# Optimization experiments

Hardware: AMD Instinct MI355X
Metric: run time of the kernel (lower is better)

## Reference

```python
import jax, jax.numpy as jnp
import numpy as np

B, S, DM = 4, 2048, 1024
H, HD = 16, 64  # num_heads, head_dimension


def setup_inputs() -> dict:
    key = jax.random.key(0)
    ks = jax.random.split(key, 11)
    s = 0.02
    return {
        "queries": jax.random.normal(ks[0], (B, S, DM), dtype=jnp.float32),
        "keys": jax.random.normal(ks[1], (B, S, DM), dtype=jnp.float32),
        "values": jax.random.normal(ks[2], (B, S, DM), dtype=jnp.float32),
        # projection params, stored [in, out] (transpose of torch Linear weight)
        "Wq": jax.random.normal(ks[3], (DM, H * HD), dtype=jnp.float32) * s,
        "bq": jnp.zeros((H * HD,), dtype=jnp.float32),
        "Wk": jax.random.normal(ks[4], (DM, H * HD), dtype=jnp.float32) * s,
        "bk": jnp.zeros((H * HD,), dtype=jnp.float32),
        "Wv": jax.random.normal(ks[5], (DM, H * HD), dtype=jnp.float32) * s,
        "bv": jnp.zeros((H * HD,), dtype=jnp.float32),
        "Wo": jax.random.normal(ks[6], (H * HD, DM), dtype=jnp.float32) * s,
        "bo": jnp.zeros((DM,), dtype=jnp.float32),
    }


def reference(queries, keys, values, Wq, bq, Wk, bk, Wv, bv, Wo, bo):
    b, s, _ = queries.shape
    # project and split heads: [b, s, H*HD] -> [b, H, s, HD]
    def split(x):
        return x.reshape(b, s, H, HD).transpose(0, 2, 1, 3)
    q = split(queries @ Wq + bq)
    k = split(keys @ Wk + bk)
    v = split(values @ Wv + bv)
    # raw scores [b, H, sq, sk]
    attn = jnp.einsum("bhqd,bhkd->bhqk", q, k)
    # FAITHFUL to source: mask is a no-op (masked_fill result discarded);
    # softmax over axis=2 (the QUERY axis), then scaled by 1/sqrt(HD) after.
    attn = jax.nn.softmax(attn, axis=2) / jnp.sqrt(jnp.float32(HD))
    out = jnp.einsum("bhqk,bhkd->bhqd", attn, v)  # [b, H, s, HD]
    out = out.transpose(0, 2, 1, 3).reshape(b, s, H * HD)
    return out @ Wo + bo
```

## Files before the change

### kernel.cpp

```cpp
#include <hip/hip_runtime.h>
#include <cstddef>


typedef unsigned short u16t;
typedef __attribute__((ext_vector_type(8))) short short8;
typedef __attribute__((ext_vector_type(4))) float floatx4;
typedef __attribute__((ext_vector_type(4))) unsigned int uintx4;

#define MFMA16(a, b, c) __builtin_amdgcn_mfma_f32_16x16x32_bf16((a), (b), (c), 0, 0, 0)
#define GLDS16(g, l)                                                        \
  __builtin_amdgcn_global_load_lds(                                         \
      (const __attribute__((address_space(1))) unsigned int*)(g),           \
      (__attribute__((address_space(3))) unsigned int*)(l), 16, 0, 0)

#if __has_builtin(__builtin_amdgcn_exp2f)
#define EXP2(x) __builtin_amdgcn_exp2f(x)
#else
#define EXP2(x) __expf(0.69314718f * (x))
#endif

static __device__ __forceinline__ u16t f2bf(float f) {
  union { float f; unsigned u; } v; v.f = f;
  unsigned r = v.u + 0x7FFFu + ((v.u >> 16) & 1u);
  return (u16t)(r >> 16);
}
static __device__ __forceinline__ unsigned pack2(float hi, float lo) {
  union { float f; unsigned u; } a, b; a.f = hi; b.f = lo;
  return __builtin_amdgcn_perm(a.u + 0x8000u, b.u + 0x8000u, 0x07060302u);
}
static __device__ __forceinline__ unsigned cvtpk(float lo, float hi) {
  unsigned r;
  asm("v_cvt_pk_bf16_f32 %0, %1, %2" : "=v"(r) : "v"(lo), "v"(hi));
  return r;
}

static __device__ __forceinline__ int swz(int row, int col) {
  return (((col >> 3) ^ (row & 7)) << 3) | (col & 7);
}

#define SEQ    2048
#define NHEAD  16
#define HDIM   64
#define DMODEL 1024

__global__ __launch_bounds__(256)
void wt_kernel(const float* __restrict__ W0, const float* __restrict__ W1,
               const float* __restrict__ W2, const float* __restrict__ W3,
               u16t* __restrict__ T0, u16t* __restrict__ T1,
               u16t* __restrict__ T2, u16t* __restrict__ T3) {
  int id = blockIdx.x * 256 + threadIdx.x;
  int wsel = id >> 17;
  int r = id & 131071;
  int n = r & 1023;
  int k0 = (r >> 10) << 3;
  const float* W = wsel == 0 ? W0 : wsel == 1 ? W1 : wsel == 2 ? W2 : W3;
  u16t* T = wsel == 0 ? T0 : wsel == 1 ? T1 : wsel == 2 ? T2 : T3;
  const float* src = W + (size_t)k0 * 1024 + n;
  float f[8];
#pragma unroll
  for (int i = 0; i < 8; ++i) f[i] = src[(size_t)i * 1024];
  uint4 p;
  p.x = pack2(f[1], f[0]); p.y = pack2(f[3], f[2]);
  p.z = pack2(f[5], f[4]); p.w = pack2(f[7], f[6]);
  *(uint4*)&T[(size_t)n * 1024 + (k0 & ~63) + swz(n, k0 & 63)] = p;
}

__global__ __launch_bounds__(256)
void cvt_kernel(const float* __restrict__ X0, const float* __restrict__ X1,
                u16t* __restrict__ T0, u16t* __restrict__ T1) {
  int id = blockIdx.x * 256 + threadIdx.x;
  int wsel = id >> 20;
  int r = id & 1048575;
  int m = r >> 7;
  int k0 = (r & 127) << 3;
  const float* X = wsel == 0 ? X0 : X1;
  u16t* T = wsel == 0 ? T0 : T1;
  const float4* src = (const float4*)(X + (size_t)m * 1024 + k0);
  float4 a = src[0], b = src[1];
  uint4 p;
  p.x = pack2(a.y, a.x); p.y = pack2(a.w, a.z);
  p.z = pack2(b.y, b.x); p.w = pack2(b.w, b.z);
  *(uint4*)&T[(size_t)m * 1024 + (k0 & ~63) + swz(m, k0 & 63)] = p;
}

template <int MODE>
__global__ __launch_bounds__(256)
void gemm_bt(const void* __restrict__ Ap0, const void* __restrict__ Ap1,
             const u16t* __restrict__ BT0, const u16t* __restrict__ BT1,
             const float* __restrict__ bias0, const float* __restrict__ bias1,
             void* __restrict__ Cp0, void* __restrict__ Cp1,
             float sc0, float sc1, const float* __restrict__ sscv) {
  constexpr int K = 1024;
  __shared__ __align__(16) u16t lA[128 * 64];
  __shared__ __align__(16) u16t lB[128 * 64];
  const int z = blockIdx.z;
  const void* Ap = z ? Ap1 : Ap0;
  const u16t* BT = z ? BT1 : BT0;
  const float* bias = z ? bias1 : bias0;
  void* Cp = z ? Cp1 : Cp0;
  const float qsc = z ? sc1 : sc0;
  const int tid = threadIdx.x;
  const int lane = tid & 63, w = tid >> 6;
  const int wm = w >> 1, wn = w & 1;
  const int lrow = lane & 15, lq = lane >> 4;
  const int raw = blockIdx.y * 8 + blockIdx.x;
  const int xcd = raw & 7, slot = raw >> 3;
  const int m0 = (xcd * 8 + (slot >> 3)) * 128;
  const int n0 = (slot & 7) * 128;

  floatx4 acc[4][4];
#pragma unroll
  for (int i = 0; i < 4; ++i)
#pragma unroll
    for (int j = 0; j < 4; ++j) acc[i][j] = {0.f, 0.f, 0.f, 0.f};

  for (int kb = 0; kb < K; kb += 64) {
    if constexpr (MODE == 2) {
      const float* Ag = (const float*)Ap;
#pragma unroll
      for (int i = 0; i < 8; ++i) {
        int e = (i * 256 + tid) * 4;
        int r = e >> 6, c = e & 63;
        const float* src = Ag + (size_t)(m0 + r) * K + kb + c;
        uint2 p;
        p.x = pack2(src[1], src[0]);
        p.y = pack2(src[3], src[2]);
        *(uint2*)&lA[r * 64 + swz(r, c)] = p;
      }
    } else {
      const u16t* Ag = (const u16t*)Ap;
#pragma unroll
      for (int i = 0; i < 4; ++i) {
        int chunk = w * 4 + i;
        int off = chunk * 1024 + lane * 16;
        int r = off >> 7, ib = off & 127;
        GLDS16(Ag + (size_t)(m0 + r) * K + kb + (ib >> 1), &lA[chunk * 512]);
      }
    }
#pragma unroll
    for (int i = 0; i < 4; ++i) {
      int chunk = w * 4 + i;
      int off = chunk * 1024 + lane * 16;
      int r = off >> 7, ib = off & 127;
      GLDS16(BT + (size_t)(n0 + r) * K + kb + (ib >> 1), &lB[chunk * 512]);
    }
    __syncthreads();
#pragma unroll
    for (int kk = 0; kk < 2; ++kk) {
      short8 af[4], bfr[4];
#pragma unroll
      for (int t = 0; t < 4; ++t) {
        int ar = wm * 64 + t * 16 + lrow;
        af[t] = *(const short8*)&lA[ar * 64 + swz(ar, kk * 32 + lq * 8)];
      }
#pragma unroll
      for (int t = 0; t < 4; ++t) {
        int br = wn * 64 + t * 16 + lrow;
        bfr[t] = *(const short8*)&lB[br * 64 + swz(br, kk * 32 + lq * 8)];
      }
#pragma unroll
      for (int i = 0; i < 4; ++i)
#pragma unroll
        for (int j = 0; j < 4; ++j)
          acc[i][j] = MFMA16(af[i], bfr[j], acc[i][j]);
    }
    __syncthreads();
  }

  float bvv[4];
#pragma unroll
  for (int j = 0; j < 4; ++j) bvv[j] = bias[n0 + wn * 64 + j * 16 + lrow];
  const int h = (n0 + wn * 64) >> 6;
#pragma unroll
  for (int i = 0; i < 4; ++i) {
#pragma unroll
    for (int r = 0; r < 4; ++r) {
      int rg = m0 + wm * 64 + i * 16 + lq * 4 + r;
      int b = rg >> 11, s = rg & 2047;
      float rs;
      if constexpr (MODE == 2) rs = sscv[(size_t)(b * NHEAD + h) * SEQ + s];
      else                     rs = qsc;
#pragma unroll
      for (int j = 0; j < 4; ++j) {
        int cg = n0 + wn * 64 + j * 16 + lrow;
        float v = acc[i][j][r] + bvv[j];
        if constexpr (MODE == 1) {
          ((float*)Cp)[(size_t)rg * 1024 + cg] = v;
        } else {
          v *= rs;
          int d = cg & 63;
          size_t bh = (size_t)(b * NHEAD + h);
          if constexpr (MODE == 0) {
            ((u16t*)Cp)[(bh * SEQ + s) * HDIM + swz(s, d)] = f2bf(v);
          } else {
            int sp = (s & ~31) | (((s >> 2) & 3) << 3) | (s & 3) |
                     (((s >> 4) & 1) << 2);
            ((u16t*)Cp)[(bh * HDIM + d) * SEQ + (s & ~127) + swz(d, sp & 127)] =
                f2bf(v);
          }
        }
      }
    }
  }
}

__global__ __launch_bounds__(256)
void stats_kernel(const u16t* __restrict__ Qb, const u16t* __restrict__ Kb,
                  float* __restrict__ ss) {
  __shared__ __align__(16) u16t lK[8192];
  __shared__ __align__(16) u16t lQ[2][8192];
  const int tid = threadIdx.x, lane = tid & 63, w = tid >> 6;
  const int lrow = lane & 15, lq = lane >> 4;
  const int bh = blockIdx.x;
  const int c0 = blockIdx.y * 128;
  const u16t* Kbase = Kb + (size_t)bh * (SEQ * HDIM);
  const u16t* Qbase = Qb + (size_t)bh * (SEQ * HDIM);

  auto stageQ = [&](int t) {
    u16t* dst = lQ[t & 1];
#pragma unroll
    for (int i = 0; i < 4; ++i) {
      int chunk = w * 4 + i;
      GLDS16(Qbase + ((size_t)t << 13) + chunk * 512 + lane * 8, &dst[chunk * 512]);
    }
  };

#pragma unroll
  for (int i = 0; i < 4; ++i) {
    int chunk = w * 4 + i;
    GLDS16(Kbase + (size_t)c0 * HDIM + chunk * 512 + lane * 8, &lK[chunk * 512]);
  }
  stageQ(0);
  stageQ(1);
  asm volatile("s_waitcnt vmcnt(4)" ::: "memory");
  __builtin_amdgcn_s_barrier();

  short8 bfK[4];
#pragma unroll
  for (int nt = 0; nt < 2; ++nt) {
    int kr = w * 32 + nt * 16 + lrow;
    bfK[nt * 2]     = *(const short8*)&lK[kr * 64 + swz(kr, lq * 8)];
    bfK[nt * 2 + 1] = *(const short8*)&lK[kr * 64 + swz(kr, lq * 8 + 32)];
  }

  float lcur[2] = {0.f, 0.f};

#pragma unroll 2
  for (int it = 0; it < 16; ++it) {
    const u16t* Q_ = lQ[it & 1];
#pragma unroll
    for (int mt = 0; mt < 8; ++mt) {
      int qr = mt * 16 + lrow;
      short8 af0 = *(const short8*)&Q_[qr * 64 + swz(qr, lq * 8)];
      short8 af1 = *(const short8*)&Q_[qr * 64 + swz(qr, lq * 8 + 32)];
#pragma unroll
      for (int nt = 0; nt < 2; ++nt) {
        floatx4 a = {0.f, 0.f, 0.f, 0.f};
        __builtin_amdgcn_s_setprio(1);
        a = MFMA16(af0, bfK[nt * 2], a);
        a = MFMA16(af1, bfK[nt * 2 + 1], a);
        __builtin_amdgcn_s_setprio(0);
        lcur[nt] += (EXP2(a[0]) + EXP2(a[1])) + (EXP2(a[2]) + EXP2(a[3]));
      }
    }
    asm volatile("s_waitcnt lgkmcnt(0)" ::: "memory");
    __builtin_amdgcn_s_barrier();
    if (it < 14) stageQ(it + 2);
    if (it < 15) {
      if (it == 14) asm volatile("s_waitcnt vmcnt(0)" ::: "memory");
      else          asm volatile("s_waitcnt vmcnt(4)" ::: "memory");
      __builtin_amdgcn_s_barrier();
    }
  }
#pragma unroll
  for (int t = 0; t < 2; ++t) {
    float ll = lcur[t];
    ll += __shfl_xor(ll, 16);
    ll += __shfl_xor(ll, 32);
    lcur[t] = ll;
  }
  if (lane < 16) {
#pragma unroll
    for (int t = 0; t < 2; ++t) {
      int col = c0 + w * 32 + t * 16 + lane;
      ss[(size_t)bh * SEQ + col] = 1.f / (8.f * lcur[t]);
    }
  }
}

__global__ __launch_bounds__(256)
void attn_kernel(const u16t* __restrict__ Qb, const u16t* __restrict__ Kb,
                 const u16t* __restrict__ Vt, u16t* __restrict__ Hout) {
  __shared__ __align__(16) u16t sK[2][8192];
  __shared__ __align__(16) u16t sV[2][8192];
  const int tid = threadIdx.x, lane = tid & 63, w = tid >> 6;
  const int lrow = lane & 15, lq = lane >> 4;
  const int bh = blockIdx.x, q0 = blockIdx.y * 256;
  const size_t hb = (size_t)bh * (SEQ * HDIM);

  auto stage = [&](int t) {
    u16t* dK = sK[t & 1];
    u16t* dV = sV[t & 1];
    const int k0 = t << 7;
#pragma unroll
    for (int i = 0; i < 4; ++i) {
      int chunk = w * 4 + i;
      GLDS16(Kb + hb + (size_t)k0 * HDIM + chunk * 512 + lane * 8, &dK[chunk * 512]);
    }
#pragma unroll
    for (int i = 0; i < 4; ++i) {
      int chunk = w * 4 + i;
      int off = chunk * 1024 + lane * 16;
      int d = off >> 8, ib = off & 255;
      GLDS16(Vt + hb + ((size_t)d << 11) + k0 + (ib >> 1), &dV[chunk * 512]);
    }
  };

  u16t* qs = (u16t*)sK;
#pragma unroll
  for (int i = 0; i < 8; ++i) {
    int chunk = w * 8 + i;
    GLDS16(Qb + hb + (size_t)q0 * HDIM + chunk * 512 + lane * 8, &qs[chunk * 512]);
  }
  __syncthreads();
  short8 bq[4][2];
#pragma unroll
  for (int j = 0; j < 4; ++j) {
    int qr = w * 64 + j * 16 + lrow;
    bq[j][0] = *(const short8*)&qs[qr * 64 + swz(qr, lq * 8)];
    bq[j][1] = *(const short8*)&qs[qr * 64 + swz(qr, lq * 8 + 32)];
  }
  __syncthreads();

  floatx4 ao[4][4];
#pragma unroll
  for (int j = 0; j < 4; ++j)
#pragma unroll
    for (int t = 0; t < 4; ++t) ao[j][t] = {0.f, 0.f, 0.f, 0.f};

  stage(0);
  stage(1);

#pragma unroll 2
  for (int kt = 0; kt < 16; ++kt) {
    if (kt < 15) asm volatile("s_waitcnt vmcnt(8)" ::: "memory");
    else         asm volatile("s_waitcnt vmcnt(0)" ::: "memory");
    __builtin_amdgcn_s_barrier();
    const u16t* K_ = sK[kt & 1];
    const u16t* V_ = sV[kt & 1];

#pragma unroll
    for (int kw = 0; kw < 4; ++kw) {
      short8 ak[2][2];
#pragma unroll
      for (int t = 0; t < 2; ++t) {
        int kr = (kw * 2 + t) * 16 + lrow;
        ak[t][0] = *(const short8*)&K_[kr * 64 + swz(kr, lq * 8)];
        ak[t][1] = *(const short8*)&K_[kr * 64 + swz(kr, lq * 8 + 32)];
      }
      short8 pa[4];
#pragma unroll
      for (int j = 0; j < 4; ++j) {
        floatx4 s0 = {0.f, 0.f, 0.f, 0.f}, s1 = {0.f, 0.f, 0.f, 0.f};
        __builtin_amdgcn_s_setprio(1);
        s0 = MFMA16(ak[0][0], bq[j][0], s0);
        s0 = MFMA16(ak[0][1], bq[j][1], s0);
        s1 = MFMA16(ak[1][0], bq[j][0], s1);
        s1 = MFMA16(ak[1][1], bq[j][1], s1);
        __builtin_amdgcn_s_setprio(0);
        uintx4 pw;
        pw[0] = cvtpk(EXP2(s0[0]), EXP2(s0[1]));
        pw[1] = cvtpk(EXP2(s0[2]), EXP2(s0[3]));
        pw[2] = cvtpk(EXP2(s1[0]), EXP2(s1[1]));
        pw[3] = cvtpk(EXP2(s1[2]), EXP2(s1[3]));
        pa[j] = __builtin_bit_cast(short8, pw);
      }
      __builtin_amdgcn_s_setprio(1);
#pragma unroll
      for (int dt = 0; dt < 4; ++dt) {
        int vr = dt * 16 + lrow;
        short8 bv = *(const short8*)&V_[vr * 128 + swz(vr, kw * 32 + lq * 8)];
#pragma unroll
        for (int j = 0; j < 4; ++j)
          ao[j][dt] = MFMA16(pa[j], bv, ao[j][dt]);
      }
      __builtin_amdgcn_s_setprio(0);
    }

    asm volatile("s_waitcnt lgkmcnt(0)" ::: "memory");
    __builtin_amdgcn_s_barrier();
    if (kt < 14) stage(kt + 2);
  }

  const int b = bh >> 4, h = bh & 15;
#pragma unroll
  for (int j = 0; j < 4; ++j)
#pragma unroll
    for (int dt = 0; dt < 4; ++dt) {
      int d = dt * 16 + lrow;
#pragma unroll
      for (int r = 0; r < 4; ++r) {
        int q = q0 + w * 64 + j * 16 + lq * 4 + r;
        Hout[((size_t)b * SEQ + q) * DMODEL + h * HDIM + swz(q, d)] = f2bf(ao[j][dt][r]);
      }
    }
}

extern "C" void kernel_launch(void* const* d_in, const int* in_sizes, int n_in,
                              void* d_out, int out_size, void* d_ws, size_t ws_size,
                              hipStream_t stream) {
  (void)in_sizes; (void)n_in; (void)out_size; (void)ws_size;
  const float* queries = (const float*)d_in[0];
  const float* keys    = (const float*)d_in[1];
  const float* values  = (const float*)d_in[2];
  const float* Wq = (const float*)d_in[3];
  const float* bq = (const float*)d_in[4];
  const float* Wk = (const float*)d_in[5];
  const float* bk = (const float*)d_in[6];
  const float* Wv = (const float*)d_in[7];
  const float* bv = (const float*)d_in[8];
  const float* Wo = (const float*)d_in[9];
  const float* bo = (const float*)d_in[10];

  char* ws = (char*)d_ws;
  const size_t MB = 1024 * 1024;
  u16t* Qb   = (u16t*)(ws + 0 * MB);
  u16t* Kb   = (u16t*)(ws + 16 * MB);
  u16t* qcv  = (u16t*)(ws + 32 * MB);
  u16t* Hout = qcv;
  u16t* kcv  = (u16t*)(ws + 48 * MB);
  u16t* Vt   = kcv;
  u16t* wqt  = (u16t*)(ws + 64 * MB);
  u16t* wkt  = (u16t*)(ws + 66 * MB);
  u16t* wvt  = (u16t*)(ws + 68 * MB);
  u16t* wot  = (u16t*)(ws + 70 * MB);
  float* ssc = (float*)(ws + 72 * MB);

  wt_kernel<<<2048, 256, 0, stream>>>(Wq, Wk, Wv, Wo, wqt, wkt, wvt, wot);

  cvt_kernel<<<8192, 256, 0, stream>>>(queries, keys, qcv, kcv);

  gemm_bt<0><<<dim3(8, 64, 2), 256, 0, stream>>>(
      qcv, kcv, wqt, wkt, bq, bk, Qb, Kb, 1.44269504f, 1.0f, nullptr);

  stats_kernel<<<dim3(64, 16), 256, 0, stream>>>(Qb, Kb, ssc);

  gemm_bt<2><<<dim3(8, 64, 1), 256, 0, stream>>>(
      values, values, wvt, wvt, bv, bv, Vt, Vt, 1.0f, 1.0f, ssc);

  attn_kernel<<<dim3(64, 8), 256, 0, stream>>>(Qb, Kb, Vt, Hout);

  gemm_bt<1><<<dim3(8, 64, 1), 256, 0, stream>>>(
      Hout, Hout, wot, wot, bo, bo, d_out, d_out, 1.0f, 1.0f, nullptr);
}
```

Measured before the change: 400.5 us.

## Prefetch K/V fragments in attention loop and simplify stats kernel staging

The attention kernel now double-buffers its per-step K and V register fragments, loading the next kw slice from LDS while MFMAs run on the current one, and asks for two waves per SIMD through launch bounds. The stats kernel drops its double-buffered async Q staging and priority hints in favour of a single buffer loaded synchronously with __syncthreads. This halves the stats kernel's LDS use, which may raise occupancy, but that kernel can no longer overlap Q loads with compute. The added fragment registers may also strain the register cap that the launch-bounds change imposes on attn_kernel.

```diff
diff --git a/kernel.cpp b/kernel.cpp
--- a/kernel.cpp
+++ b/kernel.cpp
@@ -207,8 +207,8 @@
 __global__ __launch_bounds__(256)
 void stats_kernel(const u16t* __restrict__ Qb, const u16t* __restrict__ Kb,
                   float* __restrict__ ss) {
-  __shared__ __align__(16) u16t lK[8192];
-  __shared__ __align__(16) u16t lQ[2][8192];
+  __shared__ __align__(16) u16t lK[128 * 64];
+  __shared__ __align__(16) u16t lQ[128 * 64];
   const int tid = threadIdx.x, lane = tid & 63, w = tid >> 6;
   const int lrow = lane & 15, lq = lane >> 4;
   const int bh = blockIdx.x;
@@ -216,61 +216,44 @@
   const u16t* Kbase = Kb + (size_t)bh * (SEQ * HDIM);
   const u16t* Qbase = Qb + (size_t)bh * (SEQ * HDIM);
 
-  auto stageQ = [&](int t) {
-    u16t* dst = lQ[t & 1];
-#pragma unroll
-    for (int i = 0; i < 4; ++i) {
-      int chunk = w * 4 + i;
-      GLDS16(Qbase + ((size_t)t << 13) + chunk * 512 + lane * 8, &dst[chunk * 512]);
-    }
-  };
-
 #pragma unroll
   for (int i = 0; i < 4; ++i) {
     int chunk = w * 4 + i;
     GLDS16(Kbase + (size_t)c0 * HDIM + chunk * 512 + lane * 8, &lK[chunk * 512]);
   }
-  stageQ(0);
-  stageQ(1);
-  asm volatile("s_waitcnt vmcnt(4)" ::: "memory");
-  __builtin_amdgcn_s_barrier();
 
   short8 bfK[4];
-#pragma unroll
-  for (int nt = 0; nt < 2; ++nt) {
-    int kr = w * 32 + nt * 16 + lrow;
-    bfK[nt * 2]     = *(const short8*)&lK[kr * 64 + swz(kr, lq * 8)];
-    bfK[nt * 2 + 1] = *(const short8*)&lK[kr * 64 + swz(kr, lq * 8 + 32)];
-  }
-
   float lcur[2] = {0.f, 0.f};
 
-#pragma unroll 2
-  for (int it = 0; it < 16; ++it) {
-    const u16t* Q_ = lQ[it & 1];
+  for (int q0 = 0; q0 < SEQ; q0 += 128) {
+#pragma unroll
+    for (int i = 0; i < 4; ++i) {
+      int chunk = w * 4 + i;
+      GLDS16(Qbase + (size_t)q0 * HDIM + chunk * 512 + lane * 8, &lQ[chunk * 512]);
+    }
+    __syncthreads();
+    if (q0 == 0) {
+#pragma unroll
+      for (int nt = 0; nt < 2; ++nt) {
+        int kr = w * 32 + nt * 16 + lrow;
+        bfK[nt * 2]     = *(const short8*)&lK[kr * 64 + swz(kr, lq * 8)];
+        bfK[nt * 2 + 1] = *(const short8*)&lK[kr * 64 + swz(kr, lq * 8 + 32)];
+      }
+    }
 #pragma unroll
     for (int mt = 0; mt < 8; ++mt) {
       int qr = mt * 16 + lrow;
-      short8 af0 = *(const short8*)&Q_[qr * 64 + swz(qr, lq * 8)];
-      short8 af1 = *(const short8*)&Q_[qr * 64 + swz(qr, lq * 8 + 32)];
+      short8 af0 = *(const short8*)&lQ[qr * 64 + swz(qr, lq * 8)];
+      short8 af1 = *(const short8*)&lQ[qr * 64 + swz(qr, lq * 8 + 32)];
 #pragma unroll
       for (int nt = 0; nt < 2; ++nt) {
         floatx4 a = {0.f, 0.f, 0.f, 0.f};
-        __builtin_amdgcn_s_setprio(1);
         a = MFMA16(af0, bfK[nt * 2], a);
         a = MFMA16(af1, bfK[nt * 2 + 1], a);
-        __builtin_amdgcn_s_setprio(0);
-        lcur[nt] += (EXP2(a[0]) + EXP2(a[1])) + (EXP2(a[2]) + EXP2(a[3]));
-      }
-    }
-    asm volatile("s_waitcnt lgkmcnt(0)" ::: "memory");
-    __builtin_amdgcn_s_barrier();
-    if (it < 14) stageQ(it + 2);
-    if (it < 15) {
-      if (it == 14) asm volatile("s_waitcnt vmcnt(0)" ::: "memory");
-      else          asm volatile("s_waitcnt vmcnt(4)" ::: "memory");
-      __builtin_amdgcn_s_barrier();
-    }
+        lcur[nt] += EXP2(a[0]) + EXP2(a[1]) + EXP2(a[2]) + EXP2(a[3]);
+      }
+    }
+    __syncthreads();
   }
 #pragma unroll
   for (int t = 0; t < 2; ++t) {
@@ -288,7 +271,7 @@
   }
 }
 
-__global__ __launch_bounds__(256)
+__global__ __launch_bounds__(256, 2)
 void attn_kernel(const u16t* __restrict__ Qb, const u16t* __restrict__ Kb,
                  const u16t* __restrict__ Vt, u16t* __restrict__ Hout) {
   __shared__ __align__(16) u16t sK[2][8192];
@@ -315,6 +298,21 @@
       GLDS16(Vt + hb + ((size_t)d << 11) + k0 + (ib >> 1), &dV[chunk * 512]);
     }
   };
+  auto loadK = [&](short8 dst[2][2], const u16t* K_, int kw) {
+#pragma unroll
+    for (int t = 0; t < 2; ++t) {
+      int kr = (kw * 2 + t) * 16 + lrow;
+      dst[t][0] = *(const short8*)&K_[kr * 64 + swz(kr, lq * 8)];
+      dst[t][1] = *(const short8*)&K_[kr * 64 + swz(kr, lq * 8 + 32)];
+    }
+  };
+  auto loadV = [&](short8 dst[4], const u16t* V_, int kw) {
+#pragma unroll
+    for (int dt = 0; dt < 4; ++dt) {
+      int vr = dt * 16 + lrow;
+      dst[dt] = *(const short8*)&V_[vr * 128 + swz(vr, kw * 32 + lq * 8)];
+    }
+  };
 
   u16t* qs = (u16t*)sK;
 #pragma unroll
@@ -349,24 +347,27 @@
     const u16t* K_ = sK[kt & 1];
     const u16t* V_ = sV[kt & 1];
 
+    short8 ak[2][2][2];
+    short8 bv[2][4];
+    loadK(ak[0], K_, 0);
+    loadV(bv[0], V_, 0);
+
 #pragma unroll
     for (int kw = 0; kw < 4; ++kw) {
-      short8 ak[2][2];
-#pragma unroll
-      for (int t = 0; t < 2; ++t) {
-        int kr = (kw * 2 + t) * 16 + lrow;
-        ak[t][0] = *(const short8*)&K_[kr * 64 + swz(kr, lq * 8)];
-        ak[t][1] = *(const short8*)&K_[kr * 64 + swz(kr, lq * 8 + 32)];
+      const int cb = kw & 1, nb = cb ^ 1;
+      if (kw < 3) {
+        loadK(ak[nb], K_, kw + 1);
+        loadV(bv[nb], V_, kw + 1);
       }
       short8 pa[4];
 #pragma unroll
       for (int j = 0; j < 4; ++j) {
         floatx4 s0 = {0.f, 0.f, 0.f, 0.f}, s1 = {0.f, 0.f, 0.f, 0.f};
         __builtin_amdgcn_s_setprio(1);
-        s0 = MFMA16(ak[0][0], bq[j][0], s0);
-        s0 = MFMA16(ak[0][1], bq[j][1], s0);
-        s1 = MFMA16(ak[1][0], bq[j][0], s1);
-        s1 = MFMA16(ak[1][1], bq[j][1], s1);
+        s0 = MFMA16(ak[cb][0][0], bq[j][0], s0);
+        s0 = MFMA16(ak[cb][0][1], bq[j][1], s0);
+        s1 = MFMA16(ak[cb][1][0], bq[j][0], s1);
+        s1 = MFMA16(ak[cb][1][1], bq[j][1], s1);
         __builtin_amdgcn_s_setprio(0);
         uintx4 pw;
         pw[0] = cvtpk(EXP2(s0[0]), EXP2(s0[1]));
@@ -377,13 +378,10 @@
       }
       __builtin_amdgcn_s_setprio(1);
 #pragma unroll
-      for (int dt = 0; dt < 4; ++dt) {
-        int vr = dt * 16 + lrow;
-        short8 bv = *(const short8*)&V_[vr * 128 + swz(vr, kw * 32 + lq * 8)];
+      for (int dt = 0; dt < 4; ++dt)
 #pragma unroll
         for (int j = 0; j < 4; ++j)
-          ao[j][dt] = MFMA16(pa[j], bv, ao[j][dt]);
-      }
+          ao[j][dt] = MFMA16(pa[j], bv[cb][dt], ao[j][dt]);
       __builtin_amdgcn_s_setprio(0);
     }
 
```

Measured after the change: 379.8 us. 1.05x faster.
